# Performance work log

Measured on AMD Instinct MI355X. Metric: run time of the kernel, lower is better.

Reference implementation:

```python
import jax, jax.numpy as jnp
import numpy as np

N = 50000
E = 800000
NODE_CAT = 20
EDGE_CAT = 4
NODE_CONT = 16
EDGE_CONT = 12
NODE_IN = NODE_CAT + NODE_CONT   # 36
EDGE_IN = EDGE_CAT + EDGE_CONT   # 16
C_HID = 128
C_OUT = 64
HEADS = 2
BN_EPS = 1e-5


def setup_inputs() -> dict:
    key = jax.random.key(0)
    ks = jax.random.split(key, 40)
    g = lambda i, shape, s=0.05: jax.random.normal(ks[i], shape, jnp.float32) * s
    return {
        "x_cat": jax.random.randint(ks[0], (N, 1), 0, NODE_CAT),
        "x_cont": jax.random.normal(ks[1], (N, NODE_CONT), jnp.float32),
        "edge_cat": jax.random.randint(ks[2], (E, 1), 0, EDGE_CAT),
        "edge_cont": jax.random.normal(ks[3], (E, EDGE_CONT), jnp.float32),
        "edge_index": jax.random.randint(ks[4], (2, E), 0, N),
        "node_emb": g(5, (NODE_CAT, NODE_CAT), 1.0),
        "edge_emb": g(6, (EDGE_CAT, EDGE_CAT), 1.0),
        "eps1": jnp.zeros((), jnp.float32),
        "lin_e_W1": g(7, (EDGE_IN, NODE_IN)),
        "lin_e_b1": jnp.zeros((NODE_IN,), jnp.float32),
        "nn_W1": g(8, (NODE_IN, C_HID)),
        "nn_b1": jnp.zeros((C_HID,), jnp.float32),
        "bn_g1": jnp.ones((C_HID,), jnp.float32),
        "bn_b1": jnp.zeros((C_HID,), jnp.float32),
        "bn_m1": g(9, (C_HID,)),
        "bn_v1": jax.random.uniform(ks[10], (C_HID,), jnp.float32) + 0.5,
        "eps2": jnp.zeros((), jnp.float32),
        "lin_e_W2": g(11, (EDGE_IN, C_HID)),
        "lin_e_b2": jnp.zeros((C_HID,), jnp.float32),
        "nn_W2": g(12, (C_HID, C_HID)),
        "nn_b2": jnp.zeros((C_HID,), jnp.float32),
        "bn_g2": jnp.ones((C_HID,), jnp.float32),
        "bn_b2": jnp.zeros((C_HID,), jnp.float32),
        "bn_m2": g(13, (C_HID,)),
        "bn_v2": jax.random.uniform(ks[14], (C_HID,), jnp.float32) + 0.5,
        "Wl": g(15, (C_HID, HEADS * C_OUT)),
        "bl": jnp.zeros((HEADS * C_OUT,), jnp.float32),
        "Wr": g(16, (C_HID, HEADS * C_OUT)),
        "br": jnp.zeros((HEADS * C_OUT,), jnp.float32),
        "We_g": g(17, (EDGE_IN, HEADS * C_OUT)),
        "att": g(18, (HEADS, C_OUT), 0.1),
        "gat_bias": jnp.zeros((C_OUT,), jnp.float32),
    }


def _gine(x, src, dst, ea, eps, WeW, Web, WnW, Wnb):
    # GINEConv: out = nn((1+eps)*x + sum_j relu(x_j + lin_edge(e_ij)))
    msg = jax.nn.relu(x[src] + ea @ WeW + Web)                 # [E, F]
    agg = jax.ops.segment_sum(msg, dst, num_segments=x.shape[0])
    return ((1.0 + eps) * x + agg) @ WnW + Wnb


def _bn(x, g, b, m, v):
    # BatchNorm1d in eval mode with running stats
    return g * (x - m) * jax.lax.rsqrt(v + BN_EPS) + b


def _gatv2(x, src, dst, ea, Wl, bl, Wr, br, We, att, bias):
    n = x.shape[0]
    # PyG GATv2Conv default: add self loops; self-loop edge_attr = mean of edge_attr
    loop = jnp.arange(n)
    src2 = jnp.concatenate([src, loop])
    dst2 = jnp.concatenate([dst, loop])
    ea2 = jnp.concatenate([ea, jnp.broadcast_to(ea.mean(0), (n, ea.shape[1]))], 0)
    xl = (x @ Wl + bl).reshape(n, HEADS, C_OUT)                # source transform
    xr = (x @ Wr + br).reshape(n, HEADS, C_OUT)                # target transform
    ee = (ea2 @ We).reshape(-1, HEADS, C_OUT)
    m = jax.nn.leaky_relu(xl[src2] + xr[dst2] + ee, 0.2)       # [E2, H, C]
    alpha = (m * att).sum(-1)                                  # [E2, H]
    # segment softmax over destination nodes (stable)
    amax = jax.ops.segment_max(alpha, dst2, num_segments=n)
    ex = jnp.exp(alpha - amax[dst2])
    den = jax.ops.segment_sum(ex, dst2, num_segments=n)
    a = ex / den[dst2]
    out = jax.ops.segment_sum(a[:, :, None] * xl[src2], dst2, num_segments=n)
    return out.mean(1) + bias                                  # concat=False -> head mean


def reference(x_cat, x_cont, edge_cat, edge_cont, edge_index, node_emb, edge_emb,
              eps1, lin_e_W1, lin_e_b1, nn_W1, nn_b1, bn_g1, bn_b1, bn_m1, bn_v1,
              eps2, lin_e_W2, lin_e_b2, nn_W2, nn_b2, bn_g2, bn_b2, bn_m2, bn_v2,
              Wl, bl, Wr, br, We_g, att, gat_bias):
    src, dst = edge_index[0], edge_index[1]
    x = jnp.concatenate([node_emb[x_cat[:, 0]], x_cont], -1)       # [N, 36]
    ea = jnp.concatenate([edge_emb[edge_cat[:, 0]], edge_cont], -1)  # [E, 16]
    h = _gine(x, src, dst, ea, eps1, lin_e_W1, lin_e_b1, nn_W1, nn_b1)
    h = _bn(jax.nn.relu(h), bn_g1, bn_b1, bn_m1, bn_v1)            # dropout = identity (eval)
    h = _gine(h, src, dst, ea, eps2, lin_e_W2, lin_e_b2, nn_W2, nn_b2)
    h = _bn(jax.nn.relu(h), bn_g2, bn_b2, bn_m2, bn_v2)
    return _gatv2(h, src, dst, ea, Wl, bl, Wr, br, We_g, att, gat_bias)
```

## Files before the change

### kernel.cpp

```cpp
#include <hip/hip_runtime.h>
#include <math.h>

#define N_NODES 50000
#define N_EDGES 800000
#define NODE_IN 36
#define EDGE_IN 16
#define C_HID 128
#define C_OUT 64
#define BN_EPS 1e-5f
#define DT_NT 32
#define ZSTR 136

#define SB_T 512
#define SB_N ((N_NODES + SB_T - 1) / SB_T)

#define NF_BLOCKS ((N_NODES * NODE_IN + 255) / 256)
#define DEG_BLOCKS ((N_EDGES + 255) / 256)
#define EAS_BLOCKS 512

typedef __attribute__((ext_vector_type(2))) float v2f;
typedef __attribute__((ext_vector_type(8))) short s8v;
typedef __attribute__((ext_vector_type(4))) float f4v;

__device__ __forceinline__ int rfl(int v) { return __builtin_amdgcn_readfirstlane(v); }

__device__ __forceinline__ v2f v2(float s) { v2f r; r.x = s; r.y = s; return r; }

__device__ __forceinline__ v2f unpack_bf2(unsigned u) {
    v2f r;
    r.x = __uint_as_float(u << 16);
    r.y = __uint_as_float(u & 0xFFFF0000u);
    return r;
}
__device__ __forceinline__ unsigned pack_bf2(float lo, float hi) {
    unsigned ul = __float_as_uint(lo); ul += 0x7FFF + ((ul >> 16) & 1);
    unsigned uh = __float_as_uint(hi); uh += 0x7FFF + ((uh >> 16) & 1);
    return (ul >> 16) | (uh & 0xFFFF0000u);
}
__device__ __forceinline__ ushort bf16r(float x) {
    unsigned u = __float_as_uint(x); u += 0x7FFF + ((u >> 16) & 1);
    return (ushort)(u >> 16);
}

__device__ __forceinline__ v2f sel4v(int cat, v2f a, v2f b, v2f c, v2f d) {
    v2f r = (cat == 0) ? a : b;
    r = (cat == 2) ? c : r;
    r = (cat == 3) ? d : r;
    return r;
}
__device__ __forceinline__ float sel4(int cat, float a, float b, float c, float d) {
    float r = (cat == 0) ? a : b;
    r = (cat == 2) ? c : r;
    r = (cat == 3) ? d : r;
    return r;
}

__device__ __forceinline__ float merge_pair(float x, float y, int off) {
    bool hi = (threadIdx.x & off) != 0;
    float send = hi ? x : y;
    float recv = __shfl_xor(send, off);
    return (hi ? y : x) + recv;
}

__global__ void k_prep(const int* __restrict__ xcat,
                       const float* __restrict__ xcont,
                       const float* __restrict__ node_emb,
                       const int* __restrict__ ei,
                       const int* __restrict__ ecat,
                       const float* __restrict__ econt,
                       float* __restrict__ x,
                       int* __restrict__ deg,
                       float* __restrict__ ea_sum) {
    int bb = blockIdx.x;
    if (bb < NF_BLOCKS) {
        int idx = bb * 256 + threadIdx.x;
        if (idx >= N_NODES * NODE_IN) return;
        int i = idx / NODE_IN;
        int j = idx - i * NODE_IN;
        float v;
        if (j < 20) v = node_emb[xcat[i] * 20 + j];
        else        v = xcont[i * 16 + (j - 20)];
        x[idx] = v;
        return;
    }
    if (bb < NF_BLOCKS + DEG_BLOCKS) {
        int e = (bb - NF_BLOCKS) * 256 + threadIdx.x;
        if (e >= N_EDGES) return;
        atomicAdd(deg + ei[N_EDGES + e], 1);
        return;
    }
    int blk = bb - NF_BLOCKS - DEG_BLOCKS;
    float p[12];
#pragma unroll
    for (int k = 0; k < 12; k++) p[k] = 0.f;
    float cnt[4] = {0.f, 0.f, 0.f, 0.f};
    const int stride = EAS_BLOCKS * 256;
    for (int e = blk * 256 + threadIdx.x; e < N_EDGES; e += stride) {
        int c = ecat[e];
        cnt[0] += (c == 0) ? 1.f : 0.f;
        cnt[1] += (c == 1) ? 1.f : 0.f;
        cnt[2] += (c == 2) ? 1.f : 0.f;
        cnt[3] += (c == 3) ? 1.f : 0.f;
        const float4* v4 = (const float4*)(econt + (size_t)e * 12);
        float4 a = v4[0], bq = v4[1], d = v4[2];
        p[0] += a.x;  p[1] += a.y;  p[2] += a.z;  p[3] += a.w;
        p[4] += bq.x; p[5] += bq.y; p[6] += bq.z; p[7] += bq.w;
        p[8] += d.x;  p[9] += d.y;  p[10] += d.z; p[11] += d.w;
    }
    float vals[16];
#pragma unroll
    for (int k = 0; k < 12; k++) vals[k] = p[k];
#pragma unroll
    for (int k = 0; k < 4; k++) vals[12 + k] = cnt[k];
#pragma unroll
    for (int k = 0; k < 16; k++) {
        float v = vals[k];
#pragma unroll
        for (int off = 32; off > 0; off >>= 1) v += __shfl_xor(v, off);
        vals[k] = v;
    }
    __shared__ float red[4][16];
    int wid = threadIdx.x >> 6, lane = threadIdx.x & 63;
    if (lane == 0) {
#pragma unroll
        for (int k = 0; k < 16; k++) red[wid][k] = vals[k];
    }
    __syncthreads();
    if (threadIdx.x < 16) {
        float s = red[0][threadIdx.x] + red[1][threadIdx.x] +
                  red[2][threadIdx.x] + red[3][threadIdx.x];
        atomicAdd(ea_sum + threadIdx.x, s);
    }
}

__global__ void k_wconv(const float* __restrict__ W2n, const float* __restrict__ Wl,
                        const float* __restrict__ Wr, ushort* __restrict__ wtb) {
    int idx = blockIdx.x * 256 + threadIdx.x;
    if (idx >= 3 * C_HID * C_HID) return;
    int mm = idx >> 14;
    int r = idx & 16383;
    int n = r >> 7, k = r & 127;
    const float* src = (mm == 0) ? W2n : (mm == 1 ? Wl : Wr);
    wtb[idx] = bf16r(src[k * C_HID + n]);
}

__global__ void k_scan1(const int* __restrict__ deg, int* __restrict__ bsum) {
    int i = blockIdx.x * SB_T + threadIdx.x;
    int v = (i < N_NODES) ? deg[i] : 0;
#pragma unroll
    for (int off = 32; off > 0; off >>= 1) v += __shfl_xor(v, off);
    __shared__ int red[SB_T / 64];
    int wid = threadIdx.x >> 6, lane = threadIdx.x & 63;
    if (lane == 0) red[wid] = v;
    __syncthreads();
    if (threadIdx.x == 0) {
        int s = 0;
#pragma unroll
        for (int w = 0; w < SB_T / 64; w++) s += red[w];
        bsum[blockIdx.x] = s;
    }
}

__global__ void k_scan2(const int* __restrict__ bsum, int* __restrict__ boff,
                        int* __restrict__ rowp) {
    __shared__ int s[128];
    int t = threadIdx.x;
    int v = (t < SB_N) ? bsum[t] : 0;
    s[t] = v;
    __syncthreads();
    for (int off = 1; off < 128; off <<= 1) {
        int u = (t >= off) ? s[t - off] : 0;
        __syncthreads();
        s[t] += u;
        __syncthreads();
    }
    if (t < SB_N) boff[t] = s[t] - v;
    if (t == SB_N - 1) rowp[N_NODES] = s[t];
}

__global__ void k_scan3(const int* __restrict__ deg, const int* __restrict__ boff,
                        int* __restrict__ rowp, int* __restrict__ cursor) {
    int b = blockIdx.x, t = threadIdx.x;
    int i = b * SB_T + t;
    int d = (i < N_NODES) ? deg[i] : 0;
    int lane = t & 63;
    int v = d;
#pragma unroll
    for (int off = 1; off < 64; off <<= 1) {
        int u = __shfl_up(v, off);
        if (lane >= off) v += u;
    }
    __shared__ int wsum[SB_T / 64];
    int wid = t >> 6;
    if (lane == 63) wsum[wid] = v;
    __syncthreads();
    int wo = 0;
    for (int w = 0; w < wid; w++) wo += wsum[w];
    int excl = boff[b] + wo + v - d;
    if (i < N_NODES) { rowp[i] = excl; cursor[i] = excl; }
}

__global__ void k_fill(const int* __restrict__ ei, const int* __restrict__ ecat,
                       const float* __restrict__ econt,
                       int* __restrict__ cursor, int* __restrict__ csr_ps,
                       float* __restrict__ csr_e) {
    int e = blockIdx.x * blockDim.x + threadIdx.x;
    if (e >= N_EDGES) return;
    int d = ei[N_EDGES + e];
    const float4* s4 = (const float4*)(econt + (size_t)e * 12);
    float4 a = s4[0], b = s4[1], c = s4[2];
    int pos = atomicAdd(cursor + d, 1);
    csr_ps[pos] = ei[e] | (ecat[e] << 24);
    float4* d4 = (float4*)(csr_e + (size_t)pos * 12);
    d4[0] = a; d4[1] = b; d4[2] = c;
}

__global__ void k_gine1_gather(const int* __restrict__ rowp,
                               const int* __restrict__ csr_ps,
                               const float* __restrict__ csr_e,
                               const float* __restrict__ edge_emb,
                               const float* __restrict__ W,
                               const float* __restrict__ b,
                               const float* __restrict__ x,
                               float* __restrict__ agg) {
    int i = blockIdx.x * 4 + (threadIdx.x >> 6);
    int lane = threadIdx.x & 63;
    if (i >= N_NODES) return;
    int c = (lane < NODE_IN) ? lane : (NODE_IN - 1);
    float w[12];
#pragma unroll
    for (int k = 0; k < 12; k++) w[k] = W[(4 + k) * NODE_IN + c];
    float tb[4];
#pragma unroll
    for (int q = 0; q < 4; q++) {
        float v = b[c];
#pragma unroll
        for (int k = 0; k < 4; k++) v += edge_emb[q * 4 + k] * W[k * NODE_IN + c];
        tb[q] = v;
    }
    int beg = rfl(rowp[i]), end = rfl(rowp[i + 1]);
    float acc = 0.f;
    int p = beg;
    for (; p + 4 <= end; p += 4) {
        int ps4[4];
        float4 A[4], B[4], C4[4];
        float xs[4];
#pragma unroll
        for (int bq = 0; bq < 4; bq++) {
            const float4* ec4 = (const float4*)(csr_e + (size_t)(p + bq) * 12);
            A[bq] = ec4[0]; B[bq] = ec4[1]; C4[bq] = ec4[2];
            ps4[bq] = rfl(csr_ps[p + bq]);
            xs[bq] = x[(size_t)(ps4[bq] & 0xFFFFFF) * NODE_IN + c];
        }
#pragma unroll
        for (int bq = 0; bq < 4; bq++) {
            int cat = ps4[bq] >> 24;
            float t = sel4(cat, tb[0], tb[1], tb[2], tb[3]);
            t += A[bq].x * w[0] + A[bq].y * w[1] + A[bq].z * w[2] + A[bq].w * w[3];
            t += B[bq].x * w[4] + B[bq].y * w[5] + B[bq].z * w[6] + B[bq].w * w[7];
            t += C4[bq].x * w[8] + C4[bq].y * w[9] + C4[bq].z * w[10] + C4[bq].w * w[11];
            acc += fmaxf(xs[bq] + t, 0.f);
        }
    }
    for (; p < end; ++p) {
        int ps = rfl(csr_ps[p]);
        int src = ps & 0xFFFFFF, cat = ps >> 24;
        const float4* ec4 = (const float4*)(csr_e + (size_t)p * 12);
        float4 A = ec4[0], B = ec4[1], C4 = ec4[2];
        float t = sel4(cat, tb[0], tb[1], tb[2], tb[3]);
        t += A.x * w[0] + A.y * w[1] + A.z * w[2] + A.w * w[3];
        t += B.x * w[4] + B.y * w[5] + B.z * w[6] + B.w * w[7];
        t += C4.x * w[8] + C4.y * w[9] + C4.z * w[10] + C4.w * w[11];
        acc += fmaxf(x[(size_t)src * NODE_IN + c] + t, 0.f);
    }
    if (lane < NODE_IN) agg[(size_t)i * NODE_IN + lane] = acc;
}

__global__ __launch_bounds__(256, 4) void k_gine1_node(
        const float* __restrict__ x, const float* __restrict__ agg,
        const float* __restrict__ eps_p,
        const float* __restrict__ W,
        const float* __restrict__ b, const float* __restrict__ g,
        const float* __restrict__ bb, const float* __restrict__ m,
        const float* __restrict__ v, unsigned* __restrict__ h1p) {
    __shared__ float sW[NODE_IN * C_HID];
    __shared__ float sz[DT_NT * NODE_IN];
    int tid = threadIdx.x;
    int node0 = blockIdx.x * DT_NT;
    float eps = eps_p[0];
    {
        const float4* Wv = (const float4*)W;
        float4* sWv = (float4*)sW;
        for (int t = tid; t < NODE_IN * C_HID / 4; t += 256) sWv[t] = Wv[t];
    }
    {
        int nmax = min(DT_NT, N_NODES - node0);
        int tot = nmax * NODE_IN / 4;
        const float4* xv = (const float4*)(x + (size_t)node0 * NODE_IN);
        const float4* av = (const float4*)(agg + (size_t)node0 * NODE_IN);
        float4* szv = (float4*)sz;
        float s = 1.f + eps;
        for (int t = tid; t < tot; t += 256) {
            float4 a = xv[t], c = av[t];
            float4 r;
            r.x = s * a.x + c.x; r.y = s * a.y + c.y;
            r.z = s * a.z + c.z; r.w = s * a.w + c.w;
            szv[t] = r;
        }
    }
    __syncthreads();
    int cg = tid & 15, c0 = cg * 4;
    int n0 = (tid >> 4) * 2;
    float4 bL = *(const float4*)&b[c0];
    float4 bH = *(const float4*)&b[c0 + 64];
    float accL[2][4], accH[2][4];
#pragma unroll
    for (int n = 0; n < 2; n++) {
        accL[n][0] = bL.x; accL[n][1] = bL.y; accL[n][2] = bL.z; accL[n][3] = bL.w;
        accH[n][0] = bH.x; accH[n][1] = bH.y; accH[n][2] = bH.z; accH[n][3] = bH.w;
    }
#pragma unroll 2
    for (int jb = 0; jb < NODE_IN; jb += 4) {
#pragma unroll
        for (int r = 0; r < 4; r++) {
            float4 wl = *(const float4*)&sW[(jb + r) * C_HID + c0];
            float4 wh = *(const float4*)&sW[(jb + r) * C_HID + c0 + 64];
#pragma unroll
            for (int n = 0; n < 2; n++) {
                float zz = sz[(n0 + n) * NODE_IN + jb + r];
                accL[n][0] += zz * wl.x; accL[n][1] += zz * wl.y;
                accL[n][2] += zz * wl.z; accL[n][3] += zz * wl.w;
                accH[n][0] += zz * wh.x; accH[n][1] += zz * wh.y;
                accH[n][2] += zz * wh.z; accH[n][3] += zz * wh.w;
            }
        }
    }
    float4 gL = *(const float4*)&g[c0],  gH = *(const float4*)&g[c0 + 64];
    float4 mL = *(const float4*)&m[c0],  mH = *(const float4*)&m[c0 + 64];
    float4 vL = *(const float4*)&v[c0],  vH = *(const float4*)&v[c0 + 64];
    float4 bbL = *(const float4*)&bb[c0], bbH = *(const float4*)&bb[c0 + 64];
    float scL[4] = { gL.x * rsqrtf(vL.x + BN_EPS), gL.y * rsqrtf(vL.y + BN_EPS),
                     gL.z * rsqrtf(vL.z + BN_EPS), gL.w * rsqrtf(vL.w + BN_EPS) };
    float scH[4] = { gH.x * rsqrtf(vH.x + BN_EPS), gH.y * rsqrtf(vH.y + BN_EPS),
                     gH.z * rsqrtf(vH.z + BN_EPS), gH.w * rsqrtf(vH.w + BN_EPS) };
    float mLa[4] = { mL.x, mL.y, mL.z, mL.w }, mHa[4] = { mH.x, mH.y, mH.z, mH.w };
    float bbLa[4] = { bbL.x, bbL.y, bbL.z, bbL.w }, bbHa[4] = { bbH.x, bbH.y, bbH.z, bbH.w };
#pragma unroll
    for (int n = 0; n < 2; n++) {
        int i = node0 + n0 + n;
        if (i < N_NODES) {
            uint4 o;
            unsigned* po = (unsigned*)&o;
#pragma unroll
            for (int k = 0; k < 4; k++) {
                float lo = (fmaxf(accL[n][k], 0.f) - mLa[k]) * scL[k] + bbLa[k];
                float hi = (fmaxf(accH[n][k], 0.f) - mHa[k]) * scH[k] + bbHa[k];
                po[k] = pack_bf2(lo, hi);
            }
            *(uint4*)&h1p[(size_t)i * 64 + c0] = o;
        }
    }
}

__global__ void k_gine2_gather(const int* __restrict__ rowp,
                               const int* __restrict__ csr_ps,
                               const float* __restrict__ csr_e,
                               const float* __restrict__ edge_emb,
                               const float* __restrict__ W,
                               const float* __restrict__ b,
                               const unsigned* __restrict__ h1p,
                               float2* __restrict__ aggp) {
    int i = blockIdx.x * 4 + (threadIdx.x >> 6);
    int lane = threadIdx.x & 63;
    if (i >= N_NODES) return;
    v2f w01[12];
#pragma unroll
    for (int k = 0; k < 12; k++) {
        w01[k].x = W[(4 + k) * C_HID + lane];
        w01[k].y = W[(4 + k) * C_HID + lane + 64];
    }
    v2f tb01[4];
#pragma unroll
    for (int q = 0; q < 4; q++) {
        v2f t; t.x = b[lane]; t.y = b[lane + 64];
#pragma unroll
        for (int k = 0; k < 4; k++) {
            float ev = edge_emb[q * 4 + k];
            t.x += ev * W[k * C_HID + lane];
            t.y += ev * W[k * C_HID + lane + 64];
        }
        tb01[q] = t;
    }
    const v2f zero = v2(0.f);
    int beg = rfl(rowp[i]), end = rfl(rowp[i + 1]);
    v2f acc01 = zero;
    int p = beg;
    for (; p + 4 <= end; p += 4) {
        int ps4[4];
        float4 A[4], B[4], C4[4];
        v2f xs[4];
#pragma unroll
        for (int bq = 0; bq < 4; bq++) {
            const float4* ec4 = (const float4*)(csr_e + (size_t)(p + bq) * 12);
            A[bq] = ec4[0]; B[bq] = ec4[1]; C4[bq] = ec4[2];
            ps4[bq] = rfl(csr_ps[p + bq]);
            xs[bq] = unpack_bf2(h1p[(size_t)(ps4[bq] & 0xFFFFFF) * 64 + lane]);
        }
#pragma unroll
        for (int bq = 0; bq < 4; bq++) {
            int cat = ps4[bq] >> 24;
            v2f t = sel4v(cat, tb01[0], tb01[1], tb01[2], tb01[3]);
            t = __builtin_elementwise_fma(v2(A[bq].x), w01[0], t);
            t = __builtin_elementwise_fma(v2(A[bq].y), w01[1], t);
            t = __builtin_elementwise_fma(v2(A[bq].z), w01[2], t);
            t = __builtin_elementwise_fma(v2(A[bq].w), w01[3], t);
            t = __builtin_elementwise_fma(v2(B[bq].x), w01[4], t);
            t = __builtin_elementwise_fma(v2(B[bq].y), w01[5], t);
            t = __builtin_elementwise_fma(v2(B[bq].z), w01[6], t);
            t = __builtin_elementwise_fma(v2(B[bq].w), w01[7], t);
            t = __builtin_elementwise_fma(v2(C4[bq].x), w01[8], t);
            t = __builtin_elementwise_fma(v2(C4[bq].y), w01[9], t);
            t = __builtin_elementwise_fma(v2(C4[bq].z), w01[10], t);
            t = __builtin_elementwise_fma(v2(C4[bq].w), w01[11], t);
            acc01 += __builtin_elementwise_max(xs[bq] + t, zero);
        }
    }
    for (; p < end; ++p) {
        int ps = rfl(csr_ps[p]);
        int src = ps & 0xFFFFFF, cat = ps >> 24;
        const float4* ec4 = (const float4*)(csr_e + (size_t)p * 12);
        float4 A = ec4[0], B = ec4[1], C4 = ec4[2];
        v2f xs = unpack_bf2(h1p[(size_t)src * 64 + lane]);
        v2f t = sel4v(cat, tb01[0], tb01[1], tb01[2], tb01[3]);
        t = __builtin_elementwise_fma(v2(A.x), w01[0], t);
        t = __builtin_elementwise_fma(v2(A.y), w01[1], t);
        t = __builtin_elementwise_fma(v2(A.z), w01[2], t);
        t = __builtin_elementwise_fma(v2(A.w), w01[3], t);
        t = __builtin_elementwise_fma(v2(B.x), w01[4], t);
        t = __builtin_elementwise_fma(v2(B.y), w01[5], t);
        t = __builtin_elementwise_fma(v2(B.z), w01[6], t);
        t = __builtin_elementwise_fma(v2(B.w), w01[7], t);
        t = __builtin_elementwise_fma(v2(C4.x), w01[8], t);
        t = __builtin_elementwise_fma(v2(C4.y), w01[9], t);
        t = __builtin_elementwise_fma(v2(C4.z), w01[10], t);
        t = __builtin_elementwise_fma(v2(C4.w), w01[11], t);
        acc01 += __builtin_elementwise_max(xs + t, zero);
    }
    float2 o; o.x = acc01.x; o.y = acc01.y;
    aggp[(size_t)i * 64 + lane] = o;
}

__global__ __launch_bounds__(256, 4) void k_gine2_gat0(
        const unsigned* __restrict__ h1p, const float2* __restrict__ aggp,
        const float* __restrict__ eps_p,
        const ushort* __restrict__ wtb,
        const float* __restrict__ b, const float* __restrict__ g,
        const float* __restrict__ bb, const float* __restrict__ bnm,
        const float* __restrict__ bnv,
        const float* __restrict__ bl, const float* __restrict__ br,
        const float* __restrict__ ea_sum, const float* __restrict__ edge_emb,
        const float* __restrict__ We,
        unsigned* __restrict__ xlp, float2* __restrict__ xrp,
        float* __restrict__ ee_loop) {
    __shared__ ushort zb[DT_NT * ZSTR];
    __shared__ ushort hb[DT_NT * ZSTR];
    int tid = threadIdx.x;
    int node0 = blockIdx.x * DT_NT;
    if (blockIdx.x == 0 && tid < C_HID) {
        const float inv = 1.f / (float)N_EDGES;
        float acc = 0.f;
#pragma unroll
        for (int k = 0; k < 4; k++) {
            float s = 0.f;
#pragma unroll
            for (int q = 0; q < 4; q++) s += ea_sum[12 + q] * edge_emb[q * 4 + k];
            acc += (s * inv) * We[k * C_HID + tid];
        }
#pragma unroll
        for (int k = 0; k < 12; k++)
            acc += (ea_sum[k] * inv) * We[(4 + k) * C_HID + tid];
        ee_loop[tid] = acc;
    }
    {
        int nmax = min(DT_NT, N_NODES - node0);
        float s = 1.f + eps_p[0];
        for (int t = tid; t < nmax * 64; t += 256) {
            int n = t >> 6, pp = t & 63;
            v2f h = unpack_bf2(h1p[(size_t)(node0 + n) * 64 + pp]);
            float2 a = aggp[(size_t)(node0 + n) * 64 + pp];
            unsigned pk = pack_bf2(s * h.x + a.x, s * h.y + a.y);
            zb[n * ZSTR + pp]      = (ushort)(pk & 0xFFFFu);
            zb[n * ZSTR + pp + 64] = (ushort)(pk >> 16);
        }
    }
    __syncthreads();
    int lane = tid & 63;
    int w = tid >> 6;
    int lo4 = lane & 15, hi4 = lane >> 4;
    int mt = w & 1;
    {
        int ntbase = (w >> 1) * 4;
        const ushort* zrow = &zb[(mt * 16 + lo4) * ZSTR + hi4 * 8];
        s8v afr[4];
#pragma unroll
        for (int ks = 0; ks < 4; ks++) afr[ks] = *(const s8v*)(zrow + ks * 32);
#pragma unroll
        for (int j = 0; j < 4; j++) {
            int nt = ntbase + j;
            int n = nt * 16 + lo4;
            const ushort* wrow = wtb + (size_t)n * 128 + hi4 * 8;
            f4v acc = {0.f, 0.f, 0.f, 0.f};
#pragma unroll
            for (int ks = 0; ks < 4; ks++) {
                s8v bfr = *(const s8v*)(wrow + ks * 32);
                acc = __builtin_amdgcn_mfma_f32_16x16x32_bf16(afr[ks], bfr, acc, 0, 0, 0);
            }
            float bnb = b[n];
            float sc = g[n] * rsqrtf(bnv[n] + BN_EPS);
            float mu = bnm[n], be = bb[n];
#pragma unroll
            for (int r = 0; r < 4; r++) {
                int mrow = mt * 16 + hi4 * 4 + r;
                float h2v = (fmaxf(acc[r] + bnb, 0.f) - mu) * sc + be;
                hb[mrow * ZSTR + n] = bf16r(h2v);
            }
        }
    }
    __syncthreads();
    {
        int pg = w >> 1;
        const ushort* hrow = &hb[(mt * 16 + lo4) * ZSTR + hi4 * 8];
        s8v afr[4];
#pragma unroll
        for (int ks = 0; ks < 4; ks++) afr[ks] = *(const s8v*)(hrow + ks * 32);
        for (int wsel = 0; wsel < 2; wsel++) {
            const ushort* wt = wtb + (size_t)(1 + wsel) * C_HID * C_HID;
            const float* bm = wsel ? br : bl;
            f4v accA[2], accB[2];
#pragma unroll
            for (int j = 0; j < 2; j++) {
                int cA = (pg * 2 + j) * 16 + lo4;
                const ushort* wrA = wt + (size_t)cA * 128 + hi4 * 8;
                const ushort* wrB = wt + (size_t)(cA + 64) * 128 + hi4 * 8;
                f4v aA = {0.f, 0.f, 0.f, 0.f}, aB = {0.f, 0.f, 0.f, 0.f};
#pragma unroll
                for (int ks = 0; ks < 4; ks++) {
                    s8v bA = *(const s8v*)(wrA + ks * 32);
                    s8v bB = *(const s8v*)(wrB + ks * 32);
                    aA = __builtin_amdgcn_mfma_f32_16x16x32_bf16(afr[ks], bA, aA, 0, 0, 0);
                    aB = __builtin_amdgcn_mfma_f32_16x16x32_bf16(afr[ks], bB, aB, 0, 0, 0);
                }
                accA[j] = aA; accB[j] = aB;
            }
#pragma unroll
            for (int j = 0; j < 2; j++) {
                int c = (pg * 2 + j) * 16 + lo4;
                float blo = bm[c], bhi = bm[c + 64];
#pragma unroll
                for (int r = 0; r < 4; r++) {
                    int i = node0 + mt * 16 + hi4 * 4 + r;
                    if (i < N_NODES) {
                        float lo = accA[j][r] + blo, hi = accB[j][r] + bhi;
                        if (wsel == 0) {
                            xlp[(size_t)i * 64 + c] = pack_bf2(lo, hi);
                        } else {
                            float2 o; o.x = lo; o.y = hi;
                            xrp[(size_t)i * 64 + c] = o;
                        }
                    }
                }
            }
        }
    }
}

__global__ void k_gat_fused(const int* __restrict__ rowp,
                            const int* __restrict__ csr_ps,
                            const float* __restrict__ csr_e,
                            const float* __restrict__ edge_emb,
                            const float* __restrict__ We,
                            const float* __restrict__ att,
                            const float* __restrict__ ee_loop,
                            const unsigned* __restrict__ xlp,
                            const float2* __restrict__ xrp,
                            const float* __restrict__ bias,
                            float* __restrict__ out) {
    int i = blockIdx.x * 4 + (threadIdx.x >> 6);
    int lane = threadIdx.x & 63;
    if (i >= N_NODES) return;
    v2f w01[12];
#pragma unroll
    for (int k = 0; k < 12; k++) {
        w01[k].x = We[(4 + k) * C_HID + lane];
        w01[k].y = We[(4 + k) * C_HID + lane + 64];
    }
    v2f tb01[4];
#pragma unroll
    for (int q = 0; q < 4; q++) {
        v2f t = v2(0.f);
#pragma unroll
        for (int k = 0; k < 4; k++) {
            float ev = edge_emb[q * 4 + k];
            t.x += ev * We[k * C_HID + lane];
            t.y += ev * We[k * C_HID + lane + 64];
        }
        tb01[q] = t;
    }
    v2f at01; at01.x = att[lane]; at01.y = att[lane + 64];
    v2f lp01; lp01.x = ee_loop[lane]; lp01.y = ee_loop[lane + 64];
    const v2f zero = v2(0.f);
    const v2f fifth = v2(0.2f);

    float2 xr2 = xrp[(size_t)i * 64 + lane];
    v2f xr01; xr01.x = xr2.x; xr01.y = xr2.y;
    v2f xld01 = unpack_bf2(xlp[(size_t)i * 64 + lane]);

    v2f z01 = xld01 + xr01 + lp01;
    z01 = __builtin_elementwise_max(z01, zero) +
          fifth * __builtin_elementwise_min(z01, zero);
    v2f d01 = z01 * at01;
    {
        float mq = merge_pair(d01.x, d01.y, 1);
        mq += __shfl_xor(mq, 2);
        mq += __shfl_xor(mq, 4);
        mq += __shfl_xor(mq, 8);
        mq += __shfl_xor(mq, 16);
        mq += __shfl_xor(mq, 32);
        int emqi = __float_as_int(__expf(mq));
        d01.x = __int_as_float(__builtin_amdgcn_readlane(emqi, 0));
        d01.y = __int_as_float(__builtin_amdgcn_readlane(emqi, 1));
    }
    v2f den01 = d01;
    v2f acc01 = xld01 * den01;

    int beg = rfl(rowp[i]), end = rfl(rowp[i + 1]);
    int p = beg;
    for (; p + 4 <= end; p += 4) {
        int ps4[4];
        float4 A[4], B[4], C4[4];
        v2f xs[4];
#pragma unroll
        for (int bq = 0; bq < 4; bq++) {
            const float4* ec4 = (const float4*)(csr_e + (size_t)(p + bq) * 12);
            A[bq] = ec4[0]; B[bq] = ec4[1]; C4[bq] = ec4[2];
            ps4[bq] = rfl(csr_ps[p + bq]);
            xs[bq] = unpack_bf2(xlp[(size_t)(ps4[bq] & 0xFFFFFF) * 64 + lane]);
        }
        v2f dd[4];
#pragma unroll
        for (int bq = 0; bq < 4; bq++) {
            int cat = ps4[bq] >> 24;
            v2f e = sel4v(cat, tb01[0], tb01[1], tb01[2], tb01[3]);
            e = __builtin_elementwise_fma(v2(A[bq].x), w01[0], e);
            e = __builtin_elementwise_fma(v2(A[bq].y), w01[1], e);
            e = __builtin_elementwise_fma(v2(A[bq].z), w01[2], e);
            e = __builtin_elementwise_fma(v2(A[bq].w), w01[3], e);
            e = __builtin_elementwise_fma(v2(B[bq].x), w01[4], e);
            e = __builtin_elementwise_fma(v2(B[bq].y), w01[5], e);
            e = __builtin_elementwise_fma(v2(B[bq].z), w01[6], e);
            e = __builtin_elementwise_fma(v2(B[bq].w), w01[7], e);
            e = __builtin_elementwise_fma(v2(C4[bq].x), w01[8], e);
            e = __builtin_elementwise_fma(v2(C4[bq].y), w01[9], e);
            e = __builtin_elementwise_fma(v2(C4[bq].z), w01[10], e);
            e = __builtin_elementwise_fma(v2(C4[bq].w), w01[11], e);
            v2f z = xs[bq] + xr01 + e;
            z = __builtin_elementwise_max(z, zero) +
                fifth * __builtin_elementwise_min(z, zero);
            dd[bq] = z * at01;
        }
        float m01 = merge_pair(dd[0].x, dd[0].y, 1);
        float m23 = merge_pair(dd[1].x, dd[1].y, 1);
        float m45 = merge_pair(dd[2].x, dd[2].y, 1);
        float m67 = merge_pair(dd[3].x, dd[3].y, 1);
        float n0 = merge_pair(m01, m23, 2);
        float n1 = merge_pair(m45, m67, 2);
        float q = merge_pair(n0, n1, 4);
        q += __shfl_xor(q, 8);
        q += __shfl_xor(q, 16);
        q += __shfl_xor(q, 32);
        int eqi = __float_as_int(__expf(q));
        v2f p0, p1, p2, p3;
        p0.x = __int_as_float(__builtin_amdgcn_readlane(eqi, 0));
        p0.y = __int_as_float(__builtin_amdgcn_readlane(eqi, 1));
        p1.x = __int_as_float(__builtin_amdgcn_readlane(eqi, 2));
        p1.y = __int_as_float(__builtin_amdgcn_readlane(eqi, 3));
        p2.x = __int_as_float(__builtin_amdgcn_readlane(eqi, 4));
        p2.y = __int_as_float(__builtin_amdgcn_readlane(eqi, 5));
        p3.x = __int_as_float(__builtin_amdgcn_readlane(eqi, 6));
        p3.y = __int_as_float(__builtin_amdgcn_readlane(eqi, 7));
        den01 += (p0 + p1) + (p2 + p3);
        acc01 = __builtin_elementwise_fma(p0, xs[0], acc01);
        acc01 = __builtin_elementwise_fma(p1, xs[1], acc01);
        acc01 = __builtin_elementwise_fma(p2, xs[2], acc01);
        acc01 = __builtin_elementwise_fma(p3, xs[3], acc01);
    }
    for (; p < end; ++p) {
        int ps = rfl(csr_ps[p]);
        int src = ps & 0xFFFFFF, cat = ps >> 24;
        const float4* ec4 = (const float4*)(csr_e + (size_t)p * 12);
        float4 A = ec4[0], B = ec4[1], C4 = ec4[2];
        v2f xs = unpack_bf2(xlp[(size_t)src * 64 + lane]);
        v2f e = sel4v(cat, tb01[0], tb01[1], tb01[2], tb01[3]);
        e = __builtin_elementwise_fma(v2(A.x), w01[0], e);
        e = __builtin_elementwise_fma(v2(A.y), w01[1], e);
        e = __builtin_elementwise_fma(v2(A.z), w01[2], e);
        e = __builtin_elementwise_fma(v2(A.w), w01[3], e);
        e = __builtin_elementwise_fma(v2(B.x), w01[4], e);
        e = __builtin_elementwise_fma(v2(B.y), w01[5], e);
        e = __builtin_elementwise_fma(v2(B.z), w01[6], e);
        e = __builtin_elementwise_fma(v2(B.w), w01[7], e);
        e = __builtin_elementwise_fma(v2(C4.x), w01[8], e);
        e = __builtin_elementwise_fma(v2(C4.y), w01[9], e);
        e = __builtin_elementwise_fma(v2(C4.z), w01[10], e);
        e = __builtin_elementwise_fma(v2(C4.w), w01[11], e);
        v2f z = xs + xr01 + e;
        z = __builtin_elementwise_max(z, zero) +
            fifth * __builtin_elementwise_min(z, zero);
        v2f a = z * at01;
        float mq = merge_pair(a.x, a.y, 1);
        mq += __shfl_xor(mq, 2);
        mq += __shfl_xor(mq, 4);
        mq += __shfl_xor(mq, 8);
        mq += __shfl_xor(mq, 16);
        mq += __shfl_xor(mq, 32);
        int emqi = __float_as_int(__expf(mq));
        v2f pe;
        pe.x = __int_as_float(__builtin_amdgcn_readlane(emqi, 0));
        pe.y = __int_as_float(__builtin_amdgcn_readlane(emqi, 1));
        den01 += pe;
        acc01 = __builtin_elementwise_fma(pe, xs, acc01);
    }
    out[(size_t)i * C_OUT + lane] =
        0.5f * (acc01.x / den01.x + acc01.y / den01.y) + bias[lane];
}

extern "C" void kernel_launch(void* const* d_in, const int* in_sizes, int n_in,
                              void* d_out, int out_size, void* d_ws, size_t ws_size,
                              hipStream_t stream) {
    const int*   x_cat    = (const int*)d_in[0];
    const float* x_cont   = (const float*)d_in[1];
    const int*   e_cat    = (const int*)d_in[2];
    const float* e_cont   = (const float*)d_in[3];
    const int*   ei       = (const int*)d_in[4];
    const float* node_emb = (const float*)d_in[5];
    const float* edge_emb = (const float*)d_in[6];
    const float* eps1     = (const float*)d_in[7];
    const float* W1e      = (const float*)d_in[8];
    const float* b1e      = (const float*)d_in[9];
    const float* W1n      = (const float*)d_in[10];
    const float* b1n      = (const float*)d_in[11];
    const float* g1       = (const float*)d_in[12];
    const float* bb1      = (const float*)d_in[13];
    const float* m1       = (const float*)d_in[14];
    const float* v1       = (const float*)d_in[15];
    const float* eps2     = (const float*)d_in[16];
    const float* W2e      = (const float*)d_in[17];
    const float* b2e      = (const float*)d_in[18];
    const float* W2n      = (const float*)d_in[19];
    const float* b2n      = (const float*)d_in[20];
    const float* g2       = (const float*)d_in[21];
    const float* bb2      = (const float*)d_in[22];
    const float* m2       = (const float*)d_in[23];
    const float* v2p      = (const float*)d_in[24];
    const float* Wl       = (const float*)d_in[25];
    const float* bl       = (const float*)d_in[26];
    const float* Wr       = (const float*)d_in[27];
    const float* br       = (const float*)d_in[28];
    const float* Weg      = (const float*)d_in[29];
    const float* att      = (const float*)d_in[30];
    const float* gbias    = (const float*)d_in[31];

    const size_t NF128 = (size_t)N_NODES * C_HID;

    float* A = (float*)d_ws;
    float* B = A + NF128;
    unsigned* Hb = (unsigned*)(B + NF128);
    float* ea_sum  = (float*)(Hb + (size_t)N_NODES * 64);
    float* ee_loop = ea_sum + 16;
    ushort* wtb  = (ushort*)(ee_loop + C_HID);
    float* csr_e = (float*)(wtb + 3 * C_HID * C_HID);
    int* csr_ps  = (int*)(csr_e + (size_t)N_EDGES * 12);
    int* deg     = csr_ps + N_EDGES;
    int* cursor  = deg + N_NODES;
    int* rowp    = cursor + N_NODES;
    int* bsum    = rowp + N_NODES + 1;
    int* boff    = bsum + SB_N;

    float* x = A;
    float* agg36 = B;
    float2* aggp = (float2*)B;
    float2* xrp  = (float2*)B;
    unsigned* h1p = Hb; unsigned* xlp = Hb;

    size_t need = (size_t)((char*)(boff + SB_N) - (char*)d_ws);
    if (ws_size < need) return;

    hipMemsetAsync(deg, 0, N_NODES * sizeof(int), stream);
    hipMemsetAsync(ea_sum, 0, 16 * sizeof(float), stream);

    const int EB = (N_EDGES + 255) / 256;
    const int NB4 = (N_NODES + 3) / 4;
    const int NBD = (N_NODES + DT_NT - 1) / DT_NT;
    const int WB = (3 * C_HID * C_HID + 255) / 256;

    k_wconv<<<WB, 256, 0, stream>>>(W2n, Wl, Wr, wtb);
    k_prep<<<NF_BLOCKS + DEG_BLOCKS + EAS_BLOCKS, 256, 0, stream>>>(
        x_cat, x_cont, node_emb, ei, e_cat, e_cont, x, deg, ea_sum);
    k_scan1<<<SB_N, SB_T, 0, stream>>>(deg, bsum);
    k_scan2<<<1, 128, 0, stream>>>(bsum, boff, rowp);
    k_scan3<<<SB_N, SB_T, 0, stream>>>(deg, boff, rowp, cursor);
    k_fill<<<EB, 256, 0, stream>>>(ei, e_cat, e_cont, cursor, csr_ps, csr_e);

    k_gine1_gather<<<NB4, 256, 0, stream>>>(
        rowp, csr_ps, csr_e, edge_emb, W1e, b1e, x, agg36);
    k_gine1_node<<<NBD, 256, 0, stream>>>(
        x, agg36, eps1, W1n, b1n, g1, bb1, m1, v1, h1p);
    k_gine2_gather<<<NB4, 256, 0, stream>>>(
        rowp, csr_ps, csr_e, edge_emb, W2e, b2e, h1p, aggp);

    k_gine2_gat0<<<NBD, 256, 0, stream>>>(
        h1p, aggp, eps2, wtb, b2n, g2, bb2, m2, v2p,
        bl, br, ea_sum, edge_emb, Weg, xlp, xrp, ee_loop);

    k_gat_fused<<<NB4, 256, 0, stream>>>(
        rowp, csr_ps, csr_e, edge_emb, Weg, att, ee_loop,
        xlp, xrp, gbias, (float*)d_out);
}
```

Baseline: 492.7 us.

## Fold edge-attribute sum into CSR fill and use bf16 MFMA for GINE1 node MLP

Moves the edge-attribute column-sum reduction out of the prep kernel and into the CSR fill kernel, which already reads every edge's continuous features, so the edge features are read from memory once instead of twice. The first GINE node transform now runs on bf16 MFMA 16x16x32 instructions. Its weights are pre-transposed and zero-padded to K=64 in the weight-conversion kernel, and the z tile is staged in LDS as bf16. The price is lower precision in layer-1 matmul inputs, one block-level reduction and atomic per fill block, and scattered 4-byte stores of h1p instead of 16-byte stores.

```diff
diff --git a/kernel.cpp b/kernel.cpp
--- a/kernel.cpp
+++ b/kernel.cpp
@@ -10,13 +10,16 @@
 #define BN_EPS 1e-5f
 #define DT_NT 32
 #define ZSTR 136
+#define ZS1 72
 
 #define SB_T 512
 #define SB_N ((N_NODES + SB_T - 1) / SB_T)
 
 #define NF_BLOCKS ((N_NODES * NODE_IN + 255) / 256)
 #define DEG_BLOCKS ((N_EDGES + 255) / 256)
-#define EAS_BLOCKS 512
+
+#define WTB_MAIN (3 * C_HID * C_HID)
+#define WTB_TOTAL (WTB_MAIN + C_HID * 64)
 
 typedef __attribute__((ext_vector_type(2))) float v2f;
 typedef __attribute__((ext_vector_type(8))) short s8v;
@@ -66,11 +69,8 @@
                        const float* __restrict__ xcont,
                        const float* __restrict__ node_emb,
                        const int* __restrict__ ei,
-                       const int* __restrict__ ecat,
-                       const float* __restrict__ econt,
                        float* __restrict__ x,
-                       int* __restrict__ deg,
-                       float* __restrict__ ea_sum) {
+                       int* __restrict__ deg) {
     int bb = blockIdx.x;
     if (bb < NF_BLOCKS) {
         int idx = bb * 256 + threadIdx.x;
@@ -83,65 +83,27 @@
         x[idx] = v;
         return;
     }
-    if (bb < NF_BLOCKS + DEG_BLOCKS) {
-        int e = (bb - NF_BLOCKS) * 256 + threadIdx.x;
-        if (e >= N_EDGES) return;
-        atomicAdd(deg + ei[N_EDGES + e], 1);
-        return;
-    }
-    int blk = bb - NF_BLOCKS - DEG_BLOCKS;
-    float p[12];
-#pragma unroll
-    for (int k = 0; k < 12; k++) p[k] = 0.f;
-    float cnt[4] = {0.f, 0.f, 0.f, 0.f};
-    const int stride = EAS_BLOCKS * 256;
-    for (int e = blk * 256 + threadIdx.x; e < N_EDGES; e += stride) {
-        int c = ecat[e];
-        cnt[0] += (c == 0) ? 1.f : 0.f;
-        cnt[1] += (c == 1) ? 1.f : 0.f;
-        cnt[2] += (c == 2) ? 1.f : 0.f;
-        cnt[3] += (c == 3) ? 1.f : 0.f;
-        const float4* v4 = (const float4*)(econt + (size_t)e * 12);
-        float4 a = v4[0], bq = v4[1], d = v4[2];
-        p[0] += a.x;  p[1] += a.y;  p[2] += a.z;  p[3] += a.w;
-        p[4] += bq.x; p[5] += bq.y; p[6] += bq.z; p[7] += bq.w;
-        p[8] += d.x;  p[9] += d.y;  p[10] += d.z; p[11] += d.w;
-    }
-    float vals[16];
-#pragma unroll
-    for (int k = 0; k < 12; k++) vals[k] = p[k];
-#pragma unroll
-    for (int k = 0; k < 4; k++) vals[12 + k] = cnt[k];
-#pragma unroll
-    for (int k = 0; k < 16; k++) {
-        float v = vals[k];
-#pragma unroll
-        for (int off = 32; off > 0; off >>= 1) v += __shfl_xor(v, off);
-        vals[k] = v;
-    }
-    __shared__ float red[4][16];
-    int wid = threadIdx.x >> 6, lane = threadIdx.x & 63;
-    if (lane == 0) {
-#pragma unroll
-        for (int k = 0; k < 16; k++) red[wid][k] = vals[k];
-    }
-    __syncthreads();
-    if (threadIdx.x < 16) {
-        float s = red[0][threadIdx.x] + red[1][threadIdx.x] +
-                  red[2][threadIdx.x] + red[3][threadIdx.x];
-        atomicAdd(ea_sum + threadIdx.x, s);
-    }
+    int e = (bb - NF_BLOCKS) * 256 + threadIdx.x;
+    if (e >= N_EDGES) return;
+    atomicAdd(deg + ei[N_EDGES + e], 1);
 }
 
 __global__ void k_wconv(const float* __restrict__ W2n, const float* __restrict__ Wl,
-                        const float* __restrict__ Wr, ushort* __restrict__ wtb) {
+                        const float* __restrict__ Wr, const float* __restrict__ W1n,
+                        ushort* __restrict__ wtb) {
     int idx = blockIdx.x * 256 + threadIdx.x;
-    if (idx >= 3 * C_HID * C_HID) return;
-    int mm = idx >> 14;
-    int r = idx & 16383;
-    int n = r >> 7, k = r & 127;
-    const float* src = (mm == 0) ? W2n : (mm == 1 ? Wl : Wr);
-    wtb[idx] = bf16r(src[k * C_HID + n]);
+    if (idx >= WTB_TOTAL) return;
+    if (idx < WTB_MAIN) {
+        int mm = idx >> 14;
+        int r = idx & 16383;
+        int n = r >> 7, k = r & 127;
+        const float* src = (mm == 0) ? W2n : (mm == 1 ? Wl : Wr);
+        wtb[idx] = bf16r(src[k * C_HID + n]);
+    } else {
+        int r = idx - WTB_MAIN;
+        int n = r >> 6, k = r & 63;
+        wtb[idx] = (k < NODE_IN) ? bf16r(W1n[k * C_HID + n]) : (ushort)0;
+    }
 }
 
 __global__ void k_scan1(const int* __restrict__ deg, int* __restrict__ bsum) {
@@ -203,16 +165,48 @@
 __global__ void k_fill(const int* __restrict__ ei, const int* __restrict__ ecat,
                        const float* __restrict__ econt,
                        int* __restrict__ cursor, int* __restrict__ csr_ps,
-                       float* __restrict__ csr_e) {
+                       float* __restrict__ csr_e, float* __restrict__ ea_sum) {
     int e = blockIdx.x * blockDim.x + threadIdx.x;
-    if (e >= N_EDGES) return;
-    int d = ei[N_EDGES + e];
-    const float4* s4 = (const float4*)(econt + (size_t)e * 12);
-    float4 a = s4[0], b = s4[1], c = s4[2];
-    int pos = atomicAdd(cursor + d, 1);
-    csr_ps[pos] = ei[e] | (ecat[e] << 24);
-    float4* d4 = (float4*)(csr_e + (size_t)pos * 12);
-    d4[0] = a; d4[1] = b; d4[2] = c;
+    float vals[16];
+    if (e < N_EDGES) {
+        int d = ei[N_EDGES + e];
+        const float4* s4 = (const float4*)(econt + (size_t)e * 12);
+        float4 a = s4[0], b = s4[1], c = s4[2];
+        int cat = ecat[e];
+        int pos = atomicAdd(cursor + d, 1);
+        csr_ps[pos] = ei[e] | (cat << 24);
+        float4* d4 = (float4*)(csr_e + (size_t)pos * 12);
+        d4[0] = a; d4[1] = b; d4[2] = c;
+        vals[0] = a.x;  vals[1] = a.y;  vals[2] = a.z;  vals[3] = a.w;
+        vals[4] = b.x;  vals[5] = b.y;  vals[6] = b.z;  vals[7] = b.w;
+        vals[8] = c.x;  vals[9] = c.y;  vals[10] = c.z; vals[11] = c.w;
+        vals[12] = (cat == 0) ? 1.f : 0.f;
+        vals[13] = (cat == 1) ? 1.f : 0.f;
+        vals[14] = (cat == 2) ? 1.f : 0.f;
+        vals[15] = (cat == 3) ? 1.f : 0.f;
+    } else {
+#pragma unroll
+        for (int k = 0; k < 16; k++) vals[k] = 0.f;
+    }
+#pragma unroll
+    for (int k = 0; k < 16; k++) {
+        float v = vals[k];
+#pragma unroll
+        for (int off = 32; off > 0; off >>= 1) v += __shfl_xor(v, off);
+        vals[k] = v;
+    }
+    __shared__ float red[4][16];
+    int wid = threadIdx.x >> 6, lane = threadIdx.x & 63;
+    if (lane == 0) {
+#pragma unroll
+        for (int k = 0; k < 16; k++) red[wid][k] = vals[k];
+    }
+    __syncthreads();
+    if (threadIdx.x < 16) {
+        float s = red[0][threadIdx.x] + red[1][threadIdx.x] +
+                  red[2][threadIdx.x] + red[3][threadIdx.x];
+        atomicAdd(ea_sum + threadIdx.x, s);
+    }
 }
 
 __global__ void k_gine1_gather(const int* __restrict__ rowp,
@@ -279,85 +273,64 @@
 __global__ __launch_bounds__(256, 4) void k_gine1_node(
         const float* __restrict__ x, const float* __restrict__ agg,
         const float* __restrict__ eps_p,
-        const float* __restrict__ W,
+        const ushort* __restrict__ w1t,
         const float* __restrict__ b, const float* __restrict__ g,
         const float* __restrict__ bb, const float* __restrict__ m,
         const float* __restrict__ v, unsigned* __restrict__ h1p) {
-    __shared__ float sW[NODE_IN * C_HID];
-    __shared__ float sz[DT_NT * NODE_IN];
+    __shared__ ushort zb[DT_NT * ZS1];
     int tid = threadIdx.x;
     int node0 = blockIdx.x * DT_NT;
-    float eps = eps_p[0];
-    {
-        const float4* Wv = (const float4*)W;
-        float4* sWv = (float4*)sW;
-        for (int t = tid; t < NODE_IN * C_HID / 4; t += 256) sWv[t] = Wv[t];
-    }
-    {
-        int nmax = min(DT_NT, N_NODES - node0);
-        int tot = nmax * NODE_IN / 4;
-        const float4* xv = (const float4*)(x + (size_t)node0 * NODE_IN);
-        const float4* av = (const float4*)(agg + (size_t)node0 * NODE_IN);
-        float4* szv = (float4*)sz;
-        float s = 1.f + eps;
-        for (int t = tid; t < tot; t += 256) {
-            float4 a = xv[t], c = av[t];
-            float4 r;
-            r.x = s * a.x + c.x; r.y = s * a.y + c.y;
-            r.z = s * a.z + c.z; r.w = s * a.w + c.w;
-            szv[t] = r;
-        }
+    int nmax = min(DT_NT, N_NODES - node0);
+    float s = 1.f + eps_p[0];
+    for (int t = tid; t < DT_NT * 64; t += 256) {
+        int n = t >> 6, k = t & 63;
+        float val = 0.f;
+        if (n < nmax && k < NODE_IN) {
+            size_t o = (size_t)(node0 + n) * NODE_IN + k;
+            val = s * x[o] + agg[o];
+        }
+        zb[n * ZS1 + k] = bf16r(val);
     }
     __syncthreads();
-    int cg = tid & 15, c0 = cg * 4;
-    int n0 = (tid >> 4) * 2;
-    float4 bL = *(const float4*)&b[c0];
-    float4 bH = *(const float4*)&b[c0 + 64];
-    float accL[2][4], accH[2][4];
-#pragma unroll
-    for (int n = 0; n < 2; n++) {
-        accL[n][0] = bL.x; accL[n][1] = bL.y; accL[n][2] = bL.z; accL[n][3] = bL.w;
-        accH[n][0] = bH.x; accH[n][1] = bH.y; accH[n][2] = bH.z; accH[n][3] = bH.w;
-    }
-#pragma unroll 2
-    for (int jb = 0; jb < NODE_IN; jb += 4) {
+    int lane = tid & 63, w = tid >> 6;
+    int lo4 = lane & 15, hi4 = lane >> 4;
+    int mt = w & 1, q = w >> 1;
+    const ushort* zrow = &zb[(mt * 16 + lo4) * ZS1 + hi4 * 8];
+    s8v afr[2];
+    afr[0] = *(const s8v*)(zrow);
+    afr[1] = *(const s8v*)(zrow + 32);
+    f4v accL[2], accH[2];
+#pragma unroll
+    for (int j = 0; j < 2; j++) {
+        int cL = (2 * q + j) * 16 + lo4;
+        const ushort* wrL = w1t + (size_t)cL * 64 + hi4 * 8;
+        const ushort* wrH = w1t + (size_t)(cL + 64) * 64 + hi4 * 8;
+        f4v aL = {0.f, 0.f, 0.f, 0.f}, aH = {0.f, 0.f, 0.f, 0.f};
+#pragma unroll
+        for (int ks = 0; ks < 2; ks++) {
+            s8v bL = *(const s8v*)(wrL + ks * 32);
+            s8v bH = *(const s8v*)(wrH + ks * 32);
+            aL = __builtin_amdgcn_mfma_f32_16x16x32_bf16(afr[ks], bL, aL, 0, 0, 0);
+            aH = __builtin_amdgcn_mfma_f32_16x16x32_bf16(afr[ks], bH, aH, 0, 0, 0);
+        }
+        accL[j] = aL; accH[j] = aH;
+    }
+#pragma unroll
+    for (int j = 0; j < 2; j++) {
+        int c = (2 * q + j) * 16 + lo4;
+        float bLo = b[c], bHi = b[c + 64];
+        float scLo = g[c] * rsqrtf(v[c] + BN_EPS);
+        float scHi = g[c + 64] * rsqrtf(v[c + 64] + BN_EPS);
+        float mLo = m[c], mHi = m[c + 64];
+        float beLo = bb[c], beHi = bb[c + 64];
 #pragma unroll
         for (int r = 0; r < 4; r++) {
-            float4 wl = *(const float4*)&sW[(jb + r) * C_HID + c0];
-            float4 wh = *(const float4*)&sW[(jb + r) * C_HID + c0 + 64];
-#pragma unroll
-            for (int n = 0; n < 2; n++) {
-                float zz = sz[(n0 + n) * NODE_IN + jb + r];
-                accL[n][0] += zz * wl.x; accL[n][1] += zz * wl.y;
-                accL[n][2] += zz * wl.z; accL[n][3] += zz * wl.w;
-                accH[n][0] += zz * wh.x; accH[n][1] += zz * wh.y;
-                accH[n][2] += zz * wh.z; accH[n][3] += zz * wh.w;
+            int i = node0 + mt * 16 + hi4 * 4 + r;
+            if (i < N_NODES) {
+                float lo = (fmaxf(accL[j][r] + bLo, 0.f) - mLo) * scLo + beLo;
+                float hi = (fmaxf(accH[j][r] + bHi, 0.f) - mHi) * scHi + beHi;
+                h1p[(size_t)i * 64 + c] = pack_bf2(lo, hi);
             }
-        }
-    }
-    float4 gL = *(const float4*)&g[c0],  gH = *(const float4*)&g[c0 + 64];
-    float4 mL = *(const float4*)&m[c0],  mH = *(const float4*)&m[c0 + 64];
-    float4 vL = *(const float4*)&v[c0],  vH = *(const float4*)&v[c0 + 64];
-    float4 bbL = *(const float4*)&bb[c0], bbH = *(const float4*)&bb[c0 + 64];
-    float scL[4] = { gL.x * rsqrtf(vL.x + BN_EPS), gL.y * rsqrtf(vL.y + BN_EPS),
-                     gL.z * rsqrtf(vL.z + BN_EPS), gL.w * rsqrtf(vL.w + BN_EPS) };
-    float scH[4] = { gH.x * rsqrtf(vH.x + BN_EPS), gH.y * rsqrtf(vH.y + BN_EPS),
-                     gH.z * rsqrtf(vH.z + BN_EPS), gH.w * rsqrtf(vH.w + BN_EPS) };
-    float mLa[4] = { mL.x, mL.y, mL.z, mL.w }, mHa[4] = { mH.x, mH.y, mH.z, mH.w };
-    float bbLa[4] = { bbL.x, bbL.y, bbL.z, bbL.w }, bbHa[4] = { bbH.x, bbH.y, bbH.z, bbH.w };
-#pragma unroll
-    for (int n = 0; n < 2; n++) {
-        int i = node0 + n0 + n;
-        if (i < N_NODES) {
-            uint4 o;
-            unsigned* po = (unsigned*)&o;
-#pragma unroll
-            for (int k = 0; k < 4; k++) {
-                float lo = (fmaxf(accL[n][k], 0.f) - mLa[k]) * scL[k] + bbLa[k];
-                float hi = (fmaxf(accH[n][k], 0.f) - mHa[k]) * scH[k] + bbHa[k];
-                po[k] = pack_bf2(lo, hi);
-            }
-            *(uint4*)&h1p[(size_t)i * 64 + c0] = o;
         }
     }
 }
@@ -778,7 +751,7 @@
     float* ea_sum  = (float*)(Hb + (size_t)N_NODES * 64);
     float* ee_loop = ea_sum + 16;
     ushort* wtb  = (ushort*)(ee_loop + C_HID);
-    float* csr_e = (float*)(wtb + 3 * C_HID * C_HID);
+    float* csr_e = (float*)(wtb + WTB_TOTAL);
     int* csr_ps  = (int*)(csr_e + (size_t)N_EDGES * 12);
     int* deg     = csr_ps + N_EDGES;
     int* cursor  = deg + N_NODES;
@@ -801,20 +774,20 @@
     const int EB = (N_EDGES + 255) / 256;
     const int NB4 = (N_NODES + 3) / 4;
     const int NBD = (N_NODES + DT_NT - 1) / DT_NT;
-    const int WB = (3 * C_HID * C_HID + 255) / 256;
-
-    k_wconv<<<WB, 256, 0, stream>>>(W2n, Wl, Wr, wtb);
-    k_prep<<<NF_BLOCKS + DEG_BLOCKS + EAS_BLOCKS, 256, 0, stream>>>(
-        x_cat, x_cont, node_emb, ei, e_cat, e_cont, x, deg, ea_sum);
+    const int WB = (WTB_TOTAL + 255) / 256;
+
+    k_wconv<<<WB, 256, 0, stream>>>(W2n, Wl, Wr, W1n, wtb);
+    k_prep<<<NF_BLOCKS + DEG_BLOCKS, 256, 0, stream>>>(
+        x_cat, x_cont, node_emb, ei, x, deg);
     k_scan1<<<SB_N, SB_T, 0, stream>>>(deg, bsum);
     k_scan2<<<1, 128, 0, stream>>>(bsum, boff, rowp);
     k_scan3<<<SB_N, SB_T, 0, stream>>>(deg, boff, rowp, cursor);
-    k_fill<<<EB, 256, 0, stream>>>(ei, e_cat, e_cont, cursor, csr_ps, csr_e);
+    k_fill<<<EB, 256, 0, stream>>>(ei, e_cat, e_cont, cursor, csr_ps, csr_e, ea_sum);
 
     k_gine1_gather<<<NB4, 256, 0, stream>>>(
         rowp, csr_ps, csr_e, edge_emb, W1e, b1e, x, agg36);
     k_gine1_node<<<NBD, 256, 0, stream>>>(
-        x, agg36, eps1, W1n, b1n, g1, bb1, m1, v1, h1p);
+        x, agg36, eps1, wtb + WTB_MAIN, b1n, g1, bb1, m1, v1, h1p);
     k_gine2_gather<<<NB4, 256, 0, stream>>>(
         rowp, csr_ps, csr_e, edge_emb, W2e, b2e, h1p, aggp);
 
```

Result: slower. 504.8 us (+2.5%).
